# Kernel optimization log

Measured on AMD Instinct MI355X. Metric: run time of the kernel, lower is better.

The kernel has to match this reference:

```python
import jax, jax.numpy as jnp
import numpy as np

N_NODES = 100000


def _gcn_conv(h, row, col, norm, W, b):
    # h: [N, Fin] -> [N, Fout]; standard GCN: scatter-add of normalized
    # neighbor messages after linear transform.
    h = h @ W                                   # [N, Fout]
    msg = h[col] * norm[:, None]                # [E, Fout] gather + scale
    out = jax.ops.segment_sum(msg, row, num_segments=N_NODES)
    return out + b


def setup_inputs() -> dict:
    key = jax.random.key(0)
    k1, k2, k3, k4 = jax.random.split(key, 4)
    N, E, F_IN, HID, OUT = N_NODES, 3200000, 512, 16, 40
    x = jax.random.normal(k1, (N, F_IN), dtype=jnp.float32)
    edge_index = jax.random.randint(k2, (2, E), 0, N, dtype=jnp.int64)
    W1 = jax.random.normal(k3, (F_IN, HID), dtype=jnp.float32) * (1.0 / np.sqrt(F_IN))
    b1 = jnp.zeros((HID,), dtype=jnp.float32)
    W2 = jax.random.normal(k4, (HID, OUT), dtype=jnp.float32) * (1.0 / np.sqrt(HID))
    b2 = jnp.zeros((OUT,), dtype=jnp.float32)
    return {"x": x, "edge_index": edge_index, "W1": W1, "b1": b1, "W2": W2, "b2": b2}


def reference(x, edge_index, W1, b1, W2, b2):
    N = N_NODES
    # add self-loops (GCN convention)
    loop = jnp.arange(N, dtype=edge_index.dtype)
    row = jnp.concatenate([edge_index[0], loop])  # target nodes
    col = jnp.concatenate([edge_index[1], loop])  # source nodes
    # symmetric normalization deg^-1/2 * deg^-1/2
    deg = jax.ops.segment_sum(jnp.ones_like(row, dtype=x.dtype), row, num_segments=N)
    dinv = jnp.where(deg > 0, jax.lax.rsqrt(deg), 0.0)
    norm = dinv[row] * dinv[col]                  # [E+N]

    h = _gcn_conv(x, row, col, norm, W1, b1)
    h = jax.nn.relu(h)
    out = _gcn_conv(h, row, col, norm, W2, b2)
    return out
```

## Files before the change

kernel.cpp:

```cpp
#include <hip/hip_runtime.h>

#define N_NODES 100000
#define F_IN 512
#define HID 16
#define F_OUT 40

#define NB 784
#define BSHIFT 7
#define ROWS_PB 128
#define BCAP 4608
#define CUR_PAD 16
#define APAD 17
#define PARTB 512

__global__ void k_zero(int* __restrict__ g) {
    int i = blockIdx.x * 256 + threadIdx.x;
    if (i < NB * CUR_PAD) g[i] = 0;
}

__global__ __launch_bounds__(512) void k_fat(const float* __restrict__ x,
                                             const float* __restrict__ W1,
                                             const int* __restrict__ ei, int E,
                                             int* __restrict__ gcursor,
                                             unsigned int* __restrict__ sortbuf,
                                             float* __restrict__ Hs) {
    __shared__ float smem[8 * 64 * APAD];
    int t = threadIdx.x;
    if (blockIdx.x < PARTB) {
        int* lcnt = (int*)smem;
        int* gb   = lcnt + NB;
        int epb = (E + PARTB - 1) / PARTB;
        int base = blockIdx.x * epb;
        int lim = min(base + epb, E);
        for (int cbase = base; cbase < lim; cbase += 4096) {
            int cend = min(cbase + 4096, lim);
            for (int i = t; i < NB; i += 512) lcnt[i] = 0;
            __syncthreads();
            unsigned int v[8]; int bkt[8], mi[8];
#pragma unroll
            for (int i = 0; i < 8; ++i) {
                int e = cbase + i * 512 + t;
                bkt[i] = -1;
                if (e < cend) {
                    int r = ei[e], c = ei[E + e];
                    bkt[i] = r >> BSHIFT;
                    v[i] = ((unsigned)(r & (ROWS_PB - 1)) << 17) | (unsigned)c;
                    mi[i] = atomicAdd(&lcnt[bkt[i]], 1);
                }
            }
            __syncthreads();
            for (int i = t; i < NB; i += 512)
                gb[i] = atomicAdd(&gcursor[i * CUR_PAD], lcnt[i]);
            __syncthreads();
#pragma unroll
            for (int i = 0; i < 8; ++i)
                if (bkt[i] >= 0) {
                    int idx = gb[bkt[i]] + mi[i];
                    if (idx < BCAP) sortbuf[(size_t)bkt[i] * BCAP + idx] = v[i];
                }
            __syncthreads();
        }
    } else {
        float* red = smem;
        int kc = __builtin_amdgcn_readfirstlane(t >> 6);
        int rl = t & 63;
        int bid = blockIdx.x - PARTB;
        int row = bid * 64 + rl;

        float acc[HID];
#pragma unroll
        for (int f = 0; f < HID; ++f) acc[f] = 0.0f;

        if (row < N_NODES) {
            const float* xp = x + (size_t)row * F_IN + kc * 64;
            const float* wp = W1 + kc * 64 * HID;
            float4 a0 = *reinterpret_cast<const float4*>(xp);
            float4 a1 = *reinterpret_cast<const float4*>(xp + 4);
            float4 a2 = *reinterpret_cast<const float4*>(xp + 8);
            float4 a3 = *reinterpret_cast<const float4*>(xp + 12);
            for (int k = 0; k < 64; k += 16) {
                float4 n0, n1, n2, n3;
                if (k + 16 < 64) {
                    n0 = *reinterpret_cast<const float4*>(xp + k + 16);
                    n1 = *reinterpret_cast<const float4*>(xp + k + 20);
                    n2 = *reinterpret_cast<const float4*>(xp + k + 24);
                    n3 = *reinterpret_cast<const float4*>(xp + k + 28);
                } else {
                    n0 = a0; n1 = a1; n2 = a2; n3 = a3;
                }
                float xs[16] = {a0.x, a0.y, a0.z, a0.w, a1.x, a1.y, a1.z, a1.w,
                                a2.x, a2.y, a2.z, a2.w, a3.x, a3.y, a3.z, a3.w};
#pragma unroll
                for (int kk = 0; kk < 16; ++kk) {
                    float xv = xs[kk];
#pragma unroll
                    for (int f = 0; f < HID; ++f)
                        acc[f] = fmaf(xv, wp[(k + kk) * HID + f], acc[f]);
                }
                a0 = n0; a1 = n1; a2 = n2; a3 = n3;
            }
        }
        int base = (kc * 64 + rl) * APAD;
#pragma unroll
        for (int f = 0; f < HID; ++f) red[base + f] = acc[f];
        __syncthreads();
#pragma unroll
        for (int p = 0; p < 2; ++p) {
            int o = p * 512 + t;
            int r = o >> 4, f = o & 15;
            int rg = bid * 64 + r;
            if (rg < N_NODES) {
                float s = 0.0f;
#pragma unroll
                for (int c = 0; c < 8; ++c) s += red[(c * 64 + r) * APAD + f];
                Hs[(size_t)rg * HID + f] = s;
            }
        }
    }
}

__global__ __launch_bounds__(256) void k_build(const unsigned int* __restrict__ sortbuf,
                                               const int* __restrict__ gcursor,
                                               int* __restrict__ rowptr,
                                               float* __restrict__ dinv,
                                               int* __restrict__ colv,
                                               float* __restrict__ Hs) {
    __shared__ int bb[NB];
    __shared__ int s[256];
    __shared__ int hist[ROWS_PB];
    __shared__ int rstart[ROWS_PB];
    __shared__ int cur[ROWS_PB];
    __shared__ float sdinv[ROWS_PB];
    int b = blockIdx.x, t = threadIdx.x;

    int l0 = 0, l1 = 0, l2 = 0, l3 = 0;
    if (t < 196) {
        l0 = min(gcursor[(t * 4 + 0) * CUR_PAD], BCAP);
        l1 = min(gcursor[(t * 4 + 1) * CUR_PAD], BCAP);
        l2 = min(gcursor[(t * 4 + 2) * CUR_PAD], BCAP);
        l3 = min(gcursor[(t * 4 + 3) * CUR_PAD], BCAP);
    }
    int part = l0 + l1 + l2 + l3;
    s[t] = part;
    __syncthreads();
    for (int off = 1; off < 256; off <<= 1) {
        int a = (t >= off) ? s[t - off] : 0;
        __syncthreads();
        s[t] += a;
        __syncthreads();
    }
    if (t < 196) {
        int ex = s[t] - part;
        bb[t * 4 + 0] = ex;
        bb[t * 4 + 1] = ex + l0;
        bb[t * 4 + 2] = ex + l0 + l1;
        bb[t * 4 + 3] = ex + l0 + l1 + l2;
    }
    if (t < ROWS_PB) hist[t] = 0;
    __syncthreads();
    int gbase = bb[b];
    int n = min(gcursor[b * CUR_PAD], BCAP);
    if (b == 0 && t == 0) rowptr[N_NODES] = s[255];

    const unsigned int* sb = sortbuf + (size_t)b * BCAP;
    for (int i = t; i < n; i += 256) atomicAdd(&hist[sb[i] >> 17], 1);
    __syncthreads();
    int c0 = (t < ROWS_PB) ? hist[t] : 0;
    s[t] = c0;
    __syncthreads();
    for (int off = 1; off < 256; off <<= 1) {
        int a = (t >= off) ? s[t - off] : 0;
        __syncthreads();
        s[t] += a;
        __syncthreads();
    }
    if (t < ROWS_PB) {
        int ex = s[t] - c0;
        rstart[t] = ex;
        cur[t] = 0;
        float dv = rsqrtf((float)(c0 + 1));
        sdinv[t] = dv;
        int g = b * ROWS_PB + t;
        if (g < N_NODES) {
            rowptr[g] = gbase + ex;
            dinv[g] = dv;
        }
    }
    __syncthreads();
    for (int i = t; i < n; i += 256) {
        unsigned int v = sb[i];
        int lr = v >> 17;
        int pos = atomicAdd(&cur[lr], 1);
        colv[gbase + rstart[lr] + pos] = (int)(v & 0x1FFFFu);
    }
    __syncthreads();
    for (int i = t; i < ROWS_PB * 4; i += 256) {
        int row = i >> 2, q = i & 3;
        int g = b * ROWS_PB + row;
        if (g < N_NODES) {
            float4* p = reinterpret_cast<float4*>(Hs + (size_t)g * HID + q * 4);
            float4 vv = *p;
            float dv = sdinv[row];
            vv.x *= dv; vv.y *= dv; vv.z *= dv; vv.w *= dv;
            *p = vv;
        }
    }
}

__global__ __launch_bounds__(256) void k_agg1(const int* __restrict__ rowptr,
                                              const int* __restrict__ colv,
                                              const float* __restrict__ dinv,
                                              const float* __restrict__ Hs,
                                              const float* __restrict__ b1,
                                              float* __restrict__ h1s) {
    int wid = __builtin_amdgcn_readfirstlane((blockIdx.x * 256 + threadIdx.x) >> 6);
    if (wid >= N_NODES) return;
    int lane = threadIdx.x & 63;
    int f4 = lane & 3, sub = lane >> 2;
    int beg = rowptr[wid], end = rowptr[wid + 1];
    float dr = dinv[wid];
    float4 acc = make_float4(0.f, 0.f, 0.f, 0.f);
    for (int j = beg + sub; j < end; j += 16) {
        int c = colv[j];
        float4 hv = *reinterpret_cast<const float4*>(Hs + (size_t)c * HID + f4 * 4);
        acc.x += hv.x; acc.y += hv.y; acc.z += hv.z; acc.w += hv.w;
    }
#pragma unroll
    for (int d = 4; d < 64; d <<= 1) {
        acc.x += __shfl_xor(acc.x, d);
        acc.y += __shfl_xor(acc.y, d);
        acc.z += __shfl_xor(acc.z, d);
        acc.w += __shfl_xor(acc.w, d);
    }
    if (sub == 0) {
        float4 self = *reinterpret_cast<const float4*>(Hs + (size_t)wid * HID + f4 * 4);
        float4 bb = *reinterpret_cast<const float4*>(b1 + f4 * 4);
        float4 o;
        o.x = fmaxf((acc.x + self.x) * dr + bb.x, 0.f) * dr;
        o.y = fmaxf((acc.y + self.y) * dr + bb.y, 0.f) * dr;
        o.z = fmaxf((acc.z + self.z) * dr + bb.z, 0.f) * dr;
        o.w = fmaxf((acc.w + self.w) * dr + bb.w, 0.f) * dr;
        *reinterpret_cast<float4*>(h1s + (size_t)wid * HID + f4 * 4) = o;
    }
}

__global__ __launch_bounds__(256) void k_agg2(const int* __restrict__ rowptr,
                                              const int* __restrict__ colv,
                                              const float* __restrict__ dinv,
                                              const float* __restrict__ h1s,
                                              const float* __restrict__ W2,
                                              const float* __restrict__ b2,
                                              float* __restrict__ out) {
    int wid = __builtin_amdgcn_readfirstlane((blockIdx.x * 256 + threadIdx.x) >> 6);
    if (wid >= N_NODES) return;
    int lane = threadIdx.x & 63;
    int f4 = lane & 3, sub = lane >> 2;
    int beg = rowptr[wid], end = rowptr[wid + 1];
    float dr = dinv[wid];
    float4 acc = make_float4(0.f, 0.f, 0.f, 0.f);
    for (int j = beg + sub; j < end; j += 16) {
        int c = colv[j];
        float4 hv = *reinterpret_cast<const float4*>(h1s + (size_t)c * HID + f4 * 4);
        acc.x += hv.x; acc.y += hv.y; acc.z += hv.z; acc.w += hv.w;
    }
#pragma unroll
    for (int d = 4; d < 64; d <<= 1) {
        acc.x += __shfl_xor(acc.x, d);
        acc.y += __shfl_xor(acc.y, d);
        acc.z += __shfl_xor(acc.z, d);
        acc.w += __shfl_xor(acc.w, d);
    }
    float4 self = *reinterpret_cast<const float4*>(h1s + (size_t)wid * HID + f4 * 4);
    float4 w4;
    w4.x = (acc.x + self.x) * dr;
    w4.y = (acc.y + self.y) * dr;
    w4.z = (acc.z + self.z) * dr;
    w4.w = (acc.w + self.w) * dr;
    if (lane < F_OUT) {
        float o = b2[lane];
#pragma unroll
        for (int k = 0; k < HID; ++k) {
            float comp = (k & 3) == 0 ? w4.x : (k & 3) == 1 ? w4.y
                        : (k & 3) == 2 ? w4.z : w4.w;
            float wk = __shfl(comp, k >> 2);
            o = fmaf(wk, W2[k * F_OUT + lane], o);
        }
        out[(size_t)wid * F_OUT + lane] = o;
    }
}

extern "C" void kernel_launch(void* const* d_in, const int* in_sizes, int n_in,
                              void* d_out, int out_size, void* d_ws, size_t ws_size,
                              hipStream_t stream) {
    const float* x  = (const float*)d_in[0];
    const int* ei   = (const int*)d_in[1];
    const float* W1 = (const float*)d_in[2];
    const float* b1 = (const float*)d_in[3];
    const float* W2 = (const float*)d_in[4];
    const float* b2 = (const float*)d_in[5];
    float* out = (float*)d_out;
    const int E = in_sizes[1] / 2;

    int* gcursor          = (int*)d_ws;
    int* rowptr           = gcursor + 12544;
    float* dinv           = (float*)(rowptr + 100016);
    int* colv             = (int*)(dinv + 100032);
    unsigned int* sortbuf = (unsigned int*)(colv + 3200000);
    float* h1s            = (float*)sortbuf;
    float* Hs             = (float*)(sortbuf + 3612672);

    const int nbW = (N_NODES * 64 + 255) / 256;
    const int nbG = (N_NODES + 63) / 64;

    k_zero<<<(NB * CUR_PAD + 255) / 256, 256, 0, stream>>>(gcursor);
    k_fat<<<PARTB + nbG, 512, 0, stream>>>(x, W1, ei, E, gcursor, sortbuf, Hs);
    k_build<<<NB, 256, 0, stream>>>(sortbuf, gcursor, rowptr, dinv, colv, Hs);
    k_agg1<<<nbW, 256, 0, stream>>>(rowptr, colv, dinv, Hs, b1, h1s);
    k_agg2<<<nbW, 256, 0, stream>>>(rowptr, colv, dinv, h1s, W2, b2, out);
}
```

Baseline: 218.5 us.

## Stage x tiles through LDS with coalesced loads in X@W1 path

The dense X@W1 branch of the fused kernel now loads x tiles cooperatively: 32 threads per row each read a float4, so consecutive lanes hit contiguous memory, and the tile is staged in padded shared memory in four 128-column chunks with register prefetch of the next chunk. Before, each thread streamed its own 64-float slice of one row, so a wavefront's lanes touched 64 different rows. The change targets poor coalescing on the 200MB x read, at the cost of extra __syncthreads and LDS traffic. Out-of-range rows are clamped instead of skipped.

```diff
diff --git a/kernel.cpp b/kernel.cpp
--- a/kernel.cpp
+++ b/kernel.cpp
@@ -12,6 +12,7 @@
 #define CUR_PAD 16
 #define APAD 17
 #define PARTB 512
+#define SROW 129
 
 __global__ void k_zero(int* __restrict__ g) {
     int i = blockIdx.x * 256 + threadIdx.x;
@@ -61,59 +62,69 @@
             __syncthreads();
         }
     } else {
-        float* red = smem;
-        int kc = __builtin_amdgcn_readfirstlane(t >> 6);
-        int rl = t & 63;
         int bid = blockIdx.x - PARTB;
-        int row = bid * 64 + rl;
+        int tilebase = bid * 64;
+        int srow = t >> 5;
+        int sseg = t & 31;
+        int crow = t & 63;
+        int ksub = __builtin_amdgcn_readfirstlane(t >> 6);
 
         float acc[HID];
 #pragma unroll
         for (int f = 0; f < HID; ++f) acc[f] = 0.0f;
 
-        if (row < N_NODES) {
-            const float* xp = x + (size_t)row * F_IN + kc * 64;
-            const float* wp = W1 + kc * 64 * HID;
-            float4 a0 = *reinterpret_cast<const float4*>(xp);
-            float4 a1 = *reinterpret_cast<const float4*>(xp + 4);
-            float4 a2 = *reinterpret_cast<const float4*>(xp + 8);
-            float4 a3 = *reinterpret_cast<const float4*>(xp + 12);
-            for (int k = 0; k < 64; k += 16) {
-                float4 n0, n1, n2, n3;
-                if (k + 16 < 64) {
-                    n0 = *reinterpret_cast<const float4*>(xp + k + 16);
-                    n1 = *reinterpret_cast<const float4*>(xp + k + 20);
-                    n2 = *reinterpret_cast<const float4*>(xp + k + 24);
-                    n3 = *reinterpret_cast<const float4*>(xp + k + 28);
-                } else {
-                    n0 = a0; n1 = a1; n2 = a2; n3 = a3;
+        float4 rg[4];
+#pragma unroll
+        for (int q = 0; q < 4; ++q) {
+            int r = tilebase + q * 16 + srow;
+            r = min(r, N_NODES - 1);
+            rg[q] = *reinterpret_cast<const float4*>(x + (size_t)r * F_IN + sseg * 4);
+        }
+        for (int s = 0; s < 4; ++s) {
+            __syncthreads();
+#pragma unroll
+            for (int q = 0; q < 4; ++q) {
+                int base = (q * 16 + srow) * SROW + sseg * 4;
+                smem[base + 0] = rg[q].x;
+                smem[base + 1] = rg[q].y;
+                smem[base + 2] = rg[q].z;
+                smem[base + 3] = rg[q].w;
+            }
+            if (s < 3) {
+#pragma unroll
+                for (int q = 0; q < 4; ++q) {
+                    int r = tilebase + q * 16 + srow;
+                    r = min(r, N_NODES - 1);
+                    rg[q] = *reinterpret_cast<const float4*>(
+                        x + (size_t)r * F_IN + (s + 1) * 128 + sseg * 4);
                 }
-                float xs[16] = {a0.x, a0.y, a0.z, a0.w, a1.x, a1.y, a1.z, a1.w,
-                                a2.x, a2.y, a2.z, a2.w, a3.x, a3.y, a3.z, a3.w};
-#pragma unroll
-                for (int kk = 0; kk < 16; ++kk) {
-                    float xv = xs[kk];
-#pragma unroll
-                    for (int f = 0; f < HID; ++f)
-                        acc[f] = fmaf(xv, wp[(k + kk) * HID + f], acc[f]);
-                }
-                a0 = n0; a1 = n1; a2 = n2; a3 = n3;
-            }
-        }
-        int base = (kc * 64 + rl) * APAD;
-#pragma unroll
-        for (int f = 0; f < HID; ++f) red[base + f] = acc[f];
+            }
+            __syncthreads();
+            const float* wp = W1 + (s * 128 + ksub * 16) * HID;
+            int lbase = crow * SROW + ksub * 16;
+#pragma unroll
+            for (int kk = 0; kk < 16; ++kk) {
+                float xv = smem[lbase + kk];
+#pragma unroll
+                for (int f = 0; f < HID; ++f)
+                    acc[f] = fmaf(xv, wp[kk * HID + f], acc[f]);
+            }
+        }
+        __syncthreads();
+        int rbase = (ksub * 64 + crow) * APAD;
+#pragma unroll
+        for (int f = 0; f < HID; ++f) smem[rbase + f] = acc[f];
         __syncthreads();
 #pragma unroll
         for (int p = 0; p < 2; ++p) {
             int o = p * 512 + t;
             int r = o >> 4, f = o & 15;
-            int rg = bid * 64 + r;
-            if (rg < N_NODES) {
-                float s = 0.0f;
-#pragma unroll
-                for (int c = 0; c < 8; ++c) s += red[(c * 64 + r) * APAD + f];
-                Hs[(size_t)rg * HID + f] = s;
+            int rgl = tilebase + r;
+            if (rgl < N_NODES) {
+                float sum = 0.0f;
+#pragma unroll
+                for (int c = 0; c < 8; ++c) sum += smem[(c * 64 + r) * APAD + f];
+                Hs[(size_t)rgl * HID + f] = sum;
             }
         }
     }
```

Result: faster. 211.3 us (-3.3%).
